# Optimization experiments

Hardware: AMD Instinct MI355X
Metric: run time of the kernel (lower is better)

The kernel has to match this reference:

```python
import jax, jax.numpy as jnp
import numpy as np

H_DIM = 256
NUM_HEADS = 8
HEAD_DIM = H_DIM // NUM_HEADS
BN_EPS = 1e-5
SCALE = float(np.sqrt(HEAD_DIM))


def _lens():
    # 512 graphs, ragged vertex counts cycling 32/64/96/128 -> 40960 total rows
    return np.tile(np.array([32, 64, 96, 128], dtype=np.int64), 128)


def _pad(x, lens):
    # gather ragged rows of x [total, D] into padded [B, Lmax, D]; mask [B, Lmax]
    B = lens.shape[0]
    L = int(lens.max())
    off = np.zeros(B, np.int64)
    off[1:] = np.cumsum(lens)[:-1]
    pos = np.arange(L)
    idx = off[:, None] + np.minimum(pos[None, :], lens[:, None] - 1)
    mask = pos[None, :] < lens[:, None]
    return x[jnp.asarray(idx)], jnp.asarray(mask)


def _flat_idx(lens):
    # (graph_id, position) for every real row, to un-pad back to ragged layout
    b = np.repeat(np.arange(lens.shape[0]), lens)
    i = np.concatenate([np.arange(int(l)) for l in lens])
    return jnp.asarray(b), jnp.asarray(i)


def _forward(src_h, dst_h, src_lens, dst_lens,
             W1, b1, gamma1, beta1, W2, b2, gamma2, beta2):
    src_pad, src_mask = _pad(src_h, src_lens)   # [B, Ls, H]
    dst_pad, _ = _pad(dst_h, dst_lens)          # [B, Ld, H]
    B, Ls, _ = src_pad.shape
    Ld = dst_pad.shape[1]
    # NOTE: original torch code zips self.proj but never applies it, so
    # q = raw dst, k = v = raw src.  The .view(1, head_dim, heads, N) on the
    # channel-major tensor splits feature f as f = d*NUM_HEADS + h.
    q = dst_pad.reshape(B, Ld, HEAD_DIM, NUM_HEADS)
    k = src_pad.reshape(B, Ls, HEAD_DIM, NUM_HEADS)
    v = k
    scores = jnp.einsum('bndh,bmdh->bhnm', q, k) / SCALE
    scores = jnp.where(src_mask[:, None, None, :], scores, jnp.float32(-1e30))
    attn = jax.nn.softmax(scores, axis=-1)
    out = jnp.einsum('bhnm,bmdh->bndh', attn, v).reshape(B, Ld, H_DIM)
    bidx, iidx = _flat_idx(dst_lens)
    h_msg = out[bidx, iidx]                     # [total_dst, H] ragged again
    h = dst_h
    z = jnp.concatenate([h, h_msg], axis=-1)    # [N, 2H]
    y = z @ W1.T + b1
    y = gamma1 * (y - y.mean(0)) * jax.lax.rsqrt(y.var(0) + BN_EPS) + beta1
    y = jax.nn.relu(y)
    y = y @ W2.T + b2
    y = gamma2 * (y - y.mean(0)) * jax.lax.rsqrt(y.var(0) + BN_EPS) + beta2
    return h + y


def setup_inputs() -> dict:
    lens = _lens()
    N = int(lens.sum())
    ks = jax.random.split(jax.random.key(0), 4)
    return {
        'src_h': jax.random.normal(ks[0], (N, H_DIM), jnp.float32),
        'dst_h': jax.random.normal(ks[1], (N, H_DIM), jnp.float32),
        'src_num_verts': jnp.asarray(lens, jnp.int32),
        'dst_num_verts': jnp.asarray(lens, jnp.int32),
        'W1': jax.random.normal(ks[2], (H_DIM, 2 * H_DIM), jnp.float32) / np.float32(np.sqrt(2 * H_DIM)),
        'b1': jnp.zeros((H_DIM,), jnp.float32),
        'gamma1': jnp.ones((H_DIM,), jnp.float32),
        'beta1': jnp.zeros((H_DIM,), jnp.float32),
        'W2': jax.random.normal(ks[3], (H_DIM, H_DIM), jnp.float32) / np.float32(np.sqrt(H_DIM)),
        'b2': jnp.zeros((H_DIM,), jnp.float32),
        'gamma2': jnp.ones((H_DIM,), jnp.float32),
        'beta2': jnp.zeros((H_DIM,), jnp.float32),
    }


def reference(src_h, dst_h, src_num_verts, dst_num_verts,
              W1, b1, gamma1, beta1, W2, b2, gamma2, beta2):
    # segment lengths are static metadata (torch.split takes a Python list)
    src_lens = np.asarray(jax.device_get(src_num_verts), np.int64)
    dst_lens = np.asarray(jax.device_get(dst_num_verts), np.int64)
    return _forward(src_h, dst_h, src_lens, dst_lens,
                    W1, b1, gamma1, beta1, W2, b2, gamma2, beta2)
```

## Files before the change

### kernel.cpp

```cpp
#include <hip/hip_runtime.h>
#include <cstddef>

#define H 256
#define NHEADS 8
#define HD 32

typedef __attribute__((ext_vector_type(8))) short bf16x8;
typedef __attribute__((ext_vector_type(4))) float f32x4;

__device__ __forceinline__ float bf2f(unsigned short s) {
    unsigned u = ((unsigned)s) << 16; return __builtin_bit_cast(float, u);
}
__device__ __forceinline__ float bfe2f(short s) {
    unsigned u = ((unsigned)(unsigned short)s) << 16; return __builtin_bit_cast(float, u);
}
__device__ __forceinline__ unsigned short f2bf(float x) {
    unsigned u = __builtin_bit_cast(unsigned, x);
    u += 0x7fffu + ((u >> 16) & 1u);
    return (unsigned short)(u >> 16);
}
__device__ __forceinline__ void gl_lds16(const void* g, void* l) {
    __builtin_amdgcn_global_load_lds(
        (const __attribute__((address_space(1))) void*)g,
        (__attribute__((address_space(3))) void*)l, 16, 0, 0);
}

__global__ __launch_bounds__(512) void scan_zero_kernel(
    const int* __restrict__ slen, const int* __restrict__ dlen,
    int* __restrict__ soff, int* __restrict__ doff,
    float* __restrict__ stats, int B)
{
    __shared__ int ss[512], dd[512];
    const int t = threadIdx.x;
    const int sv = (t < B) ? slen[t] : 0;
    const int dv = (t < B) ? dlen[t] : 0;
    ss[t] = sv; dd[t] = dv;
    __syncthreads();
    for (int o = 1; o < 512; o <<= 1) {
        int a = (t >= o) ? ss[t - o] : 0;
        int b = (t >= o) ? dd[t - o] : 0;
        __syncthreads();
        ss[t] += a; dd[t] += b;
        __syncthreads();
    }
    if (t < B) { soff[t] = ss[t] - sv; doff[t] = dd[t] - dv; }
    stats[t] = 0.f;
    stats[t + 512] = 0.f;
}

__global__ __launch_bounds__(256) void prepass_kernel(
    const float* __restrict__ src, const float* __restrict__ dst,
    unsigned short* __restrict__ KT, unsigned short* __restrict__ VT2,
    unsigned short* __restrict__ QT, int N)
{
    __shared__ unsigned short pl[8 * 64 * 40];
    const int t = threadIdx.x;
    const int rb = blockIdx.x * 64;
    const int isrc = (blockIdx.y == 0);
    const float* __restrict__ in = isrc ? src : dst;
    unsigned short* __restrict__ T = isrc ? KT : QT;
    #pragma unroll
    for (int i = 0; i < 16; ++i) {
        const int idx = t + i * 256;
        const int row = idx >> 6, f4 = idx & 63;
        const float4 v = ((const float4*)in)[(size_t)(rb + row) * 64 + f4];
        const int f0 = f4 * 4, h0 = f0 & 7, d = f0 >> 3;
        pl[(h0 + 0) * 2560 + row * 40 + d] = f2bf(v.x);
        pl[(h0 + 1) * 2560 + row * 40 + d] = f2bf(v.y);
        pl[(h0 + 2) * 2560 + row * 40 + d] = f2bf(v.z);
        pl[(h0 + 3) * 2560 + row * 40 + d] = f2bf(v.w);
    }
    __syncthreads();
    #pragma unroll
    for (int i = 0; i < 8; ++i) {
        const int idx = t + i * 256;
        const int h = idx >> 8, rem = idx & 255, row = rem >> 2, c = rem & 3;
        const bf16x8 val = *(const bf16x8*)&pl[h * 2560 + row * 40 + c * 8];
        *(bf16x8*)&T[(size_t)(h * N + rb + row) * 32 + c * 8] = val;
    }
    if (isrc) {
        #pragma unroll
        for (int i = 0; i < 8; ++i) {
            const int idx = t + i * 256;
            const int h = idx >> 8, rem = idx & 255, d = rem >> 3, nc = rem & 7;
            unsigned short tmp[8];
            #pragma unroll
            for (int j = 0; j < 8; ++j) tmp[j] = pl[h * 2560 + (nc * 8 + j) * 40 + d];
            ushort4 lo, hi;
            lo.x = tmp[0]; lo.y = tmp[1]; lo.z = tmp[2]; lo.w = tmp[3];
            hi.x = tmp[4]; hi.y = tmp[5]; hi.z = tmp[6]; hi.w = tmp[7];
            *(ushort4*)&VT2[(size_t)(h * 32 + d) * N + rb + nc * 8] = lo;
            *(ushort4*)&VT2[(size_t)(h * 32 + d) * N + rb + nc * 8 + 4] = hi;
        }
    }
}

__global__ __launch_bounds__(256) void cvtW_kernel(
    const float* __restrict__ W1, const float* __restrict__ W2,
    unsigned short* __restrict__ W1p, unsigned short* __restrict__ W2bf)
{
    const int idx = blockIdx.x * 256 + threadIdx.x;
    if (idx < 131072) {
        const int kp = idx & 511, c = idx >> 9;
        const int half = kp >> 8, r = kp & 255, hh = r >> 5, d = r & 31;
        W1p[(size_t)c * 512 + kp] = f2bf(W1[(size_t)c * 512 + half * 256 + d * 8 + hh]);
    } else {
        const int i2 = idx - 131072;
        W2bf[i2] = f2bf(W2[i2]);
    }
}

template<int LS>
__device__ __forceinline__ void attn_body(
    const unsigned short* __restrict__ KT, const unsigned short* __restrict__ QT,
    const unsigned short* __restrict__ VT2, unsigned short* __restrict__ OT,
    unsigned short* __restrict__ Ps, int N, int so, int df, int Ld, int h, int lane)
{
    constexpr int MT = LS / 16, CH = LS / 32;
    const int lr = lane & 15, lq = lane >> 4;
    const float iscale = 0.17677669529663687f;

    bf16x8 kf[MT];
    #pragma unroll
    for (int mt = 0; mt < MT; ++mt)
        kf[mt] = *(const bf16x8*)&KT[(size_t)(h * N + so + mt * 16 + lr) * 32 + lq * 8];
    bf16x8 vf[CH][2];
    #pragma unroll
    for (int c = 0; c < CH; ++c)
        #pragma unroll
        for (int dt = 0; dt < 2; ++dt)
            vf[c][dt] = *(const bf16x8*)&VT2[(size_t)(h * 32 + dt * 16 + lr) * N + so + c * 32 + lq * 8];

    const int NT = Ld >> 4;
    for (int nt = 0; nt < NT; ++nt) {
        const bf16x8 qf = *(const bf16x8*)&QT[(size_t)(h * N + df + nt * 16 + lr) * 32 + lq * 8];
        f32x4 s[MT];
        #pragma unroll
        for (int mt = 0; mt < MT; ++mt) {
            f32x4 z = {0.f, 0.f, 0.f, 0.f};
            s[mt] = __builtin_amdgcn_mfma_f32_16x16x32_bf16(kf[mt], qf, z, 0, 0, 0);
        }
        float mx = -INFINITY;
        #pragma unroll
        for (int mt = 0; mt < MT; ++mt)
            mx = fmaxf(mx, fmaxf(fmaxf(s[mt][0], s[mt][1]), fmaxf(s[mt][2], s[mt][3])));
        mx = fmaxf(mx, __shfl_xor(mx, 16));
        mx = fmaxf(mx, __shfl_xor(mx, 32));
        const float mxi = mx * iscale;
        float sum = 0.f;
        #pragma unroll
        for (int mt = 0; mt < MT; ++mt) {
            #pragma unroll
            for (int r = 0; r < 4; ++r) {
                const float e = __expf(s[mt][r] * iscale - mxi);
                s[mt][r] = e; sum += e;
            }
        }
        sum += __shfl_xor(sum, 16);
        sum += __shfl_xor(sum, 32);
        const float rinv = 1.f / sum;
        #pragma unroll
        for (int mt = 0; mt < MT; ++mt) {
            uint2 p;
            p.x = ((unsigned)f2bf(s[mt][0])) | (((unsigned)f2bf(s[mt][1])) << 16);
            p.y = ((unsigned)f2bf(s[mt][2])) | (((unsigned)f2bf(s[mt][3])) << 16);
            *(uint2*)&Ps[lr * 136 + mt * 16 + lq * 4] = p;
        }
        __asm__ volatile("" ::: "memory");
        __builtin_amdgcn_wave_barrier();
        f32x4 o0 = {0.f, 0.f, 0.f, 0.f}, o1 = {0.f, 0.f, 0.f, 0.f};
        #pragma unroll
        for (int c = 0; c < CH; ++c) {
            const bf16x8 pa = *(const bf16x8*)&Ps[lr * 136 + c * 32 + lq * 8];
            o0 = __builtin_amdgcn_mfma_f32_16x16x32_bf16(pa, vf[c][0], o0, 0, 0, 0);
            o1 = __builtin_amdgcn_mfma_f32_16x16x32_bf16(pa, vf[c][1], o1, 0, 0, 0);
        }
        __asm__ volatile("" ::: "memory");
        __builtin_amdgcn_wave_barrier();
        #pragma unroll
        for (int r = 0; r < 4; ++r) {
            const float rv = __shfl(rinv, lq * 4 + r);
            const int row = df + nt * 16 + lq * 4 + r;
            OT[(size_t)(h * N + row) * 32 + lr]      = f2bf(o0[r] * rv);
            OT[(size_t)(h * N + row) * 32 + 16 + lr] = f2bf(o1[r] * rv);
        }
    }
}

__global__ __launch_bounds__(256) void attn_mfma(
    const unsigned short* __restrict__ KT, const unsigned short* __restrict__ QT,
    const unsigned short* __restrict__ VT2, unsigned short* __restrict__ OT,
    const int* __restrict__ soff, const int* __restrict__ doff,
    const int* __restrict__ slen, const int* __restrict__ dlen, int N)
{
    __shared__ unsigned short Ps[4][16 * 136];
    const int b = blockIdx.x >> 1, half = blockIdx.x & 1;
    const int w = threadIdx.x >> 6, lane = threadIdx.x & 63;
    const int h = half * 4 + w;
    const int Ls = slen[b], Ld = dlen[b], so = soff[b], df = doff[b];
    switch (Ls) {
        case 32:  attn_body<32> (KT, QT, VT2, OT, Ps[w], N, so, df, Ld, h, lane); break;
        case 64:  attn_body<64> (KT, QT, VT2, OT, Ps[w], N, so, df, Ld, h, lane); break;
        case 96:  attn_body<96> (KT, QT, VT2, OT, Ps[w], N, so, df, Ld, h, lane); break;
        default:  attn_body<128>(KT, QT, VT2, OT, Ps[w], N, so, df, Ld, h, lane); break;
    }
}

__global__ __launch_bounds__(256) void gemm1_mfma(
    const unsigned short* __restrict__ QT, const unsigned short* __restrict__ OT,
    const unsigned short* __restrict__ W, const float* __restrict__ bias,
    unsigned short* __restrict__ out, float* __restrict__ sum, float* __restrict__ sq,
    int N)
{
    __shared__ unsigned short Abuf[2][8 * 512];
    __shared__ unsigned short Bbuf[2][8 * 512];
    const int tid = threadIdx.x;
    const int w = tid >> 6, lane = tid & 63;
    const int rowBase = blockIdx.y * 128, colBase = blockIdx.x * 128;
    const int lr = lane & 15, lq = lane >> 4;
    const int wm = w >> 1, wn = w & 1;

    f32x4 acc[4][4];
    #pragma unroll
    for (int i = 0; i < 4; ++i)
        #pragma unroll
        for (int j = 0; j < 4; ++j) { f32x4 z = {0.f, 0.f, 0.f, 0.f}; acc[i][j] = z; }

    auto stage = [&](int ks, int bi) {
        const unsigned short* __restrict__ Ap = (ks < 8) ? QT : OT;
        const int hh = ks & 7;
        #pragma unroll
        for (int s = 0; s < 2; ++s) {
            const int sub = 2 * w + s;
            gl_lds16(Ap + (size_t)(hh * N + rowBase + sub * 16 + lr) * 32 + lq * 8,
                     &Abuf[bi][sub * 512]);
            gl_lds16(W + (size_t)(colBase + sub * 16 + lr) * 512 + ks * 32 + lq * 8,
                     &Bbuf[bi][sub * 512]);
        }
    };
    auto compute = [&](int bi) {
        bf16x8 af[4], bfr[4];
        #pragma unroll
        for (int i = 0; i < 4; ++i) af[i] = *(const bf16x8*)&Abuf[bi][(wm * 4 + i) * 512 + lane * 8];
        #pragma unroll
        for (int j = 0; j < 4; ++j) bfr[j] = *(const bf16x8*)&Bbuf[bi][(wn * 4 + j) * 512 + lane * 8];
        #pragma unroll
        for (int i = 0; i < 4; ++i)
            #pragma unroll
            for (int j = 0; j < 4; ++j)
                acc[i][j] = __builtin_amdgcn_mfma_f32_16x16x32_bf16(af[i], bfr[j], acc[i][j], 0, 0, 0);
    };

    stage(0, 0);
    __syncthreads();
    for (int ks = 0; ks < 16; ks += 2) {
        stage(ks + 1, 1);
        compute(0);
        __syncthreads();
        if (ks + 2 < 16) stage(ks + 2, 0);
        compute(1);
        __syncthreads();
    }

    const int col0 = colBase + wn * 64;
    #pragma unroll
    for (int j = 0; j < 4; ++j) {
        const int col = col0 + j * 16 + lr;
        const float bv = bias[col];
        float cs = 0.f, cq = 0.f;
        #pragma unroll
        for (int i = 0; i < 4; ++i) {
            const int row0 = rowBase + wm * 64 + i * 16 + lq * 4;
            #pragma unroll
            for (int r = 0; r < 4; ++r) {
                const float v = acc[i][j][r] + bv;
                cs += v; cq += v * v;
                out[(size_t)(row0 + r) * 256 + col] = f2bf(v);
            }
        }
        cs += __shfl_xor(cs, 16); cs += __shfl_xor(cs, 32);
        cq += __shfl_xor(cq, 16); cq += __shfl_xor(cq, 32);
        if (lq == 0) { atomicAdd(&sum[col], cs); atomicAdd(&sq[col], cq); }
    }
}

__global__ __launch_bounds__(256) void gemm2_mfma(
    const unsigned short* __restrict__ A2,
    const unsigned short* __restrict__ W, const float* __restrict__ bias,
    unsigned short* __restrict__ out, float* __restrict__ sum, float* __restrict__ sq)
{
    __shared__ unsigned short Abuf[2][8 * 512];
    __shared__ unsigned short Bbuf[2][8 * 512];
    const int tid = threadIdx.x;
    const int w = tid >> 6, lane = tid & 63;
    const int rowBase = blockIdx.y * 128, colBase = blockIdx.x * 128;
    const int lr = lane & 15, lq = lane >> 4;
    const int wm = w >> 1, wn = w & 1;

    f32x4 acc[4][4];
    #pragma unroll
    for (int i = 0; i < 4; ++i)
        #pragma unroll
        for (int j = 0; j < 4; ++j) { f32x4 z = {0.f, 0.f, 0.f, 0.f}; acc[i][j] = z; }

    auto stage = [&](int ks, int bi) {
        #pragma unroll
        for (int s = 0; s < 2; ++s) {
            const int sub = 2 * w + s;
            gl_lds16(A2 + (size_t)(rowBase + sub * 16 + lr) * 256 + ks * 32 + lq * 8,
                     &Abuf[bi][sub * 512]);
            gl_lds16(W + (size_t)(colBase + sub * 16 + lr) * 256 + ks * 32 + lq * 8,
                     &Bbuf[bi][sub * 512]);
        }
    };
    auto compute = [&](int bi) {
        bf16x8 af[4], bfr[4];
        #pragma unroll
        for (int i = 0; i < 4; ++i) af[i] = *(const bf16x8*)&Abuf[bi][(wm * 4 + i) * 512 + lane * 8];
        #pragma unroll
        for (int j = 0; j < 4; ++j) bfr[j] = *(const bf16x8*)&Bbuf[bi][(wn * 4 + j) * 512 + lane * 8];
        #pragma unroll
        for (int i = 0; i < 4; ++i)
            #pragma unroll
            for (int j = 0; j < 4; ++j)
                acc[i][j] = __builtin_amdgcn_mfma_f32_16x16x32_bf16(af[i], bfr[j], acc[i][j], 0, 0, 0);
    };

    stage(0, 0);
    __syncthreads();
    for (int ks = 0; ks < 8; ks += 2) {
        stage(ks + 1, 1);
        compute(0);
        __syncthreads();
        if (ks + 2 < 8) stage(ks + 2, 0);
        compute(1);
        __syncthreads();
    }

    const int col0 = colBase + wn * 64;
    #pragma unroll
    for (int j = 0; j < 4; ++j) {
        const int col = col0 + j * 16 + lr;
        const float bv = bias[col];
        float cs = 0.f, cq = 0.f;
        #pragma unroll
        for (int i = 0; i < 4; ++i) {
            const int row0 = rowBase + wm * 64 + i * 16 + lq * 4;
            #pragma unroll
            for (int r = 0; r < 4; ++r) {
                const float v = acc[i][j][r] + bv;
                cs += v; cq += v * v;
                out[(size_t)(row0 + r) * 256 + col] = f2bf(v);
            }
        }
        cs += __shfl_xor(cs, 16); cs += __shfl_xor(cs, 32);
        cq += __shfl_xor(cq, 16); cq += __shfl_xor(cq, 32);
        if (lq == 0) { atomicAdd(&sum[col], cs); atomicAdd(&sq[col], cq); }
    }
}

__global__ __launch_bounds__(256) void bnrelu_kernel(
    const unsigned short* __restrict__ y1,
    const float* __restrict__ sum, const float* __restrict__ sq,
    const float* __restrict__ gamma, const float* __restrict__ beta,
    unsigned short* __restrict__ out, int n8, float invN)
{
    const int i = blockIdx.x * 256 + threadIdx.x;
    if (i >= n8) return;
    const int j0 = (i & 31) * 8;
    const bf16x8 yv = ((const bf16x8*)y1)[i];
    short res[8];
    #pragma unroll
    for (int j = 0; j < 8; ++j) {
        const float mean = sum[j0 + j] * invN;
        const float var  = sq[j0 + j] * invN - mean * mean;
        const float rstd = rsqrtf(var + 1e-5f);
        const float sc = gamma[j0 + j] * rstd;
        const float sh = beta[j0 + j] - mean * sc;
        res[j] = (short)f2bf(fmaxf(bfe2f(yv[j]) * sc + sh, 0.f));
    }
    bf16x8 o;
    #pragma unroll
    for (int j = 0; j < 8; ++j) o[j] = res[j];
    ((bf16x8*)out)[i] = o;
}

__global__ __launch_bounds__(256) void epilogue_kernel(
    const float* __restrict__ dst, const unsigned short* __restrict__ y2,
    const float* __restrict__ sum, const float* __restrict__ sq,
    const float* __restrict__ gamma, const float* __restrict__ beta,
    float* __restrict__ out, int n8, float invN)
{
    const int i = blockIdx.x * 256 + threadIdx.x;
    if (i >= n8) return;
    const int j0 = (i & 31) * 8;
    const bf16x8 yv = ((const bf16x8*)y2)[i];
    const float4 d0 = ((const float4*)dst)[2 * i];
    const float4 d1 = ((const float4*)dst)[2 * i + 1];
    float o[8];
    const float dv[8] = {d0.x, d0.y, d0.z, d0.w, d1.x, d1.y, d1.z, d1.w};
    #pragma unroll
    for (int j = 0; j < 8; ++j) {
        const float mean = sum[j0 + j] * invN;
        const float var  = sq[j0 + j] * invN - mean * mean;
        const float rstd = rsqrtf(var + 1e-5f);
        const float sc = gamma[j0 + j] * rstd;
        const float sh = beta[j0 + j] - mean * sc;
        o[j] = dv[j] + bfe2f(yv[j]) * sc + sh;
    }
    float4 o0, o1;
    o0.x = o[0]; o0.y = o[1]; o0.z = o[2]; o0.w = o[3];
    o1.x = o[4]; o1.y = o[5]; o1.z = o[6]; o1.w = o[7];
    ((float4*)out)[2 * i]     = o0;
    ((float4*)out)[2 * i + 1] = o1;
}

extern "C" void kernel_launch(void* const* d_in, const int* in_sizes, int n_in,
                              void* d_out, int out_size, void* d_ws, size_t ws_size,
                              hipStream_t stream)
{
    const float* src_h  = (const float*)d_in[0];
    const float* dst_h  = (const float*)d_in[1];
    const int*   slen   = (const int*)d_in[2];
    const int*   dlen   = (const int*)d_in[3];
    const float* W1     = (const float*)d_in[4];
    const float* b1     = (const float*)d_in[5];
    const float* gamma1 = (const float*)d_in[6];
    const float* beta1  = (const float*)d_in[7];
    const float* W2     = (const float*)d_in[8];
    const float* b2     = (const float*)d_in[9];
    const float* gamma2 = (const float*)d_in[10];
    const float* beta2  = (const float*)d_in[11];
    float* out = (float*)d_out;

    const int N = in_sizes[1] / H;
    const int B = in_sizes[2];

    char* base = (char*)d_ws;
    int*   soff   = (int*)(base + 0);
    int*   doff   = (int*)(base + 2048);
    float* stats  = (float*)(base + 4096);
    unsigned short* W1p  = (unsigned short*)(base + 16384);
    unsigned short* W2bf = (unsigned short*)(base + 16384 + 262144);
    const size_t S = (size_t)N * H * sizeof(unsigned short);
    char* big = base + (1 << 20);
    unsigned short* KT  = (unsigned short*)(big);
    unsigned short* VT2 = (unsigned short*)(big + S);
    unsigned short* QT  = (unsigned short*)(big + 2 * S);
    unsigned short* OT  = (unsigned short*)(big + 3 * S);
    unsigned short* y1bf = KT;
    unsigned short* a2   = VT2;
    unsigned short* y2bf = QT;

    const float invN = 1.0f / (float)N;

    scan_zero_kernel<<<1, 512, 0, stream>>>(slen, dlen, soff, doff, stats, B);

    prepass_kernel<<<dim3(N / 64, 2), 256, 0, stream>>>(src_h, dst_h, KT, VT2, QT, N);
    cvtW_kernel<<<768, 256, 0, stream>>>(W1, W2, W1p, W2bf);

    attn_mfma<<<B * 2, 256, 0, stream>>>(KT, QT, VT2, OT, soff, doff, slen, dlen, N);

    dim3 ggrid(H / 128, N / 128);
    gemm1_mfma<<<ggrid, 256, 0, stream>>>(QT, OT, W1p, b1, y1bf, stats + 0, stats + 256, N);

    const int n8 = N * H / 8;
    bnrelu_kernel<<<(n8 + 255) / 256, 256, 0, stream>>>(
        y1bf, stats + 0, stats + 256, gamma1, beta1, a2, n8, invN);

    gemm2_mfma<<<ggrid, 256, 0, stream>>>(a2, W2bf, b2, y2bf, stats + 512, stats + 768);

    epilogue_kernel<<<(n8 + 255) / 256, 256, 0, stream>>>(
        dst_h, y2bf, stats + 512, stats + 768, gamma2, beta2, out, n8, invN);
}
```

Before: 281.2 us.

## Shrink GEMM row tiles, prefetch Q fragments, reorder attention blocks, pad LDS planes

Both GEMM kernels now use 64x128 tiles instead of 128x128, doubling the grid, with each wave covering all 64 rows and 32 columns. The aim is better occupancy and more blocks across CUs. The attention kernel maps blocks so the largest graphs are scheduled first, and it prefetches the next Q fragment one iteration ahead. The prepass pads the LDS head-plane stride to cut bank conflicts and writes VT2 with one 16-byte store. Smaller GEMM tiles lower per-block reuse of W, so W traffic through LDS goes up.

Measured after the change: 276.0 us. Within noise of the previous version (-1.8%).

```diff
diff --git a/kernel.cpp b/kernel.cpp
--- a/kernel.cpp
+++ b/kernel.cpp
@@ -48,12 +48,13 @@
     stats[t + 512] = 0.f;
 }
 
+#define PS 2568
 __global__ __launch_bounds__(256) void prepass_kernel(
     const float* __restrict__ src, const float* __restrict__ dst,
     unsigned short* __restrict__ KT, unsigned short* __restrict__ VT2,
     unsigned short* __restrict__ QT, int N)
 {
-    __shared__ unsigned short pl[8 * 64 * 40];
+    __shared__ unsigned short pl[8 * PS];
     const int t = threadIdx.x;
     const int rb = blockIdx.x * 64;
     const int isrc = (blockIdx.y == 0);
@@ -65,17 +66,17 @@
         const int row = idx >> 6, f4 = idx & 63;
         const float4 v = ((const float4*)in)[(size_t)(rb + row) * 64 + f4];
         const int f0 = f4 * 4, h0 = f0 & 7, d = f0 >> 3;
-        pl[(h0 + 0) * 2560 + row * 40 + d] = f2bf(v.x);
-        pl[(h0 + 1) * 2560 + row * 40 + d] = f2bf(v.y);
-        pl[(h0 + 2) * 2560 + row * 40 + d] = f2bf(v.z);
-        pl[(h0 + 3) * 2560 + row * 40 + d] = f2bf(v.w);
+        pl[(h0 + 0) * PS + row * 40 + d] = f2bf(v.x);
+        pl[(h0 + 1) * PS + row * 40 + d] = f2bf(v.y);
+        pl[(h0 + 2) * PS + row * 40 + d] = f2bf(v.z);
+        pl[(h0 + 3) * PS + row * 40 + d] = f2bf(v.w);
     }
     __syncthreads();
     #pragma unroll
     for (int i = 0; i < 8; ++i) {
         const int idx = t + i * 256;
         const int h = idx >> 8, rem = idx & 255, row = rem >> 2, c = rem & 3;
-        const bf16x8 val = *(const bf16x8*)&pl[h * 2560 + row * 40 + c * 8];
+        const bf16x8 val = *(const bf16x8*)&pl[h * PS + row * 40 + c * 8];
         *(bf16x8*)&T[(size_t)(h * N + rb + row) * 32 + c * 8] = val;
     }
     if (isrc) {
@@ -83,14 +84,11 @@
         for (int i = 0; i < 8; ++i) {
             const int idx = t + i * 256;
             const int h = idx >> 8, rem = idx & 255, d = rem >> 3, nc = rem & 7;
-            unsigned short tmp[8];
-            #pragma unroll
-            for (int j = 0; j < 8; ++j) tmp[j] = pl[h * 2560 + (nc * 8 + j) * 40 + d];
-            ushort4 lo, hi;
-            lo.x = tmp[0]; lo.y = tmp[1]; lo.z = tmp[2]; lo.w = tmp[3];
-            hi.x = tmp[4]; hi.y = tmp[5]; hi.z = tmp[6]; hi.w = tmp[7];
-            *(ushort4*)&VT2[(size_t)(h * 32 + d) * N + rb + nc * 8] = lo;
-            *(ushort4*)&VT2[(size_t)(h * 32 + d) * N + rb + nc * 8 + 4] = hi;
+            bf16x8 v8;
+            #pragma unroll
+            for (int j = 0; j < 8; ++j)
+                v8[j] = (short)pl[h * PS + (nc * 8 + j) * 40 + d];
+            *(bf16x8*)&VT2[(size_t)(h * 32 + d) * N + rb + nc * 8] = v8;
         }
     }
 }
@@ -132,8 +130,11 @@
             vf[c][dt] = *(const bf16x8*)&VT2[(size_t)(h * 32 + dt * 16 + lr) * N + so + c * 32 + lq * 8];
 
     const int NT = Ld >> 4;
+    bf16x8 qf = *(const bf16x8*)&QT[(size_t)(h * N + df + lr) * 32 + lq * 8];
     for (int nt = 0; nt < NT; ++nt) {
-        const bf16x8 qf = *(const bf16x8*)&QT[(size_t)(h * N + df + nt * 16 + lr) * 32 + lq * 8];
+        bf16x8 qn = qf;
+        if (nt + 1 < NT)
+            qn = *(const bf16x8*)&QT[(size_t)(h * N + df + (nt + 1) * 16 + lr) * 32 + lq * 8];
         f32x4 s[MT];
         #pragma unroll
         for (int mt = 0; mt < MT; ++mt) {
@@ -184,6 +185,7 @@
             OT[(size_t)(h * N + row) * 32 + lr]      = f2bf(o0[r] * rv);
             OT[(size_t)(h * N + row) * 32 + 16 + lr] = f2bf(o1[r] * rv);
         }
+        qf = qn;
     }
 }
 
@@ -194,7 +196,9 @@
     const int* __restrict__ slen, const int* __restrict__ dlen, int N)
 {
     __shared__ unsigned short Ps[4][16 * 136];
-    const int b = blockIdx.x >> 1, half = blockIdx.x & 1;
+    const int i = blockIdx.x >> 1, half = blockIdx.x & 1;
+    const int grp = i >> 7, j = i & 127;
+    const int b = 4 * j + (3 - grp);
     const int w = threadIdx.x >> 6, lane = threadIdx.x & 63;
     const int h = half * 4 + w;
     const int Ls = slen[b], Ld = dlen[b], so = soff[b], df = doff[b];
@@ -212,42 +216,41 @@
     unsigned short* __restrict__ out, float* __restrict__ sum, float* __restrict__ sq,
     int N)
 {
-    __shared__ unsigned short Abuf[2][8 * 512];
+    __shared__ unsigned short Abuf[2][4 * 512];
     __shared__ unsigned short Bbuf[2][8 * 512];
     const int tid = threadIdx.x;
     const int w = tid >> 6, lane = tid & 63;
-    const int rowBase = blockIdx.y * 128, colBase = blockIdx.x * 128;
+    const int rowBase = blockIdx.y * 64, colBase = blockIdx.x * 128;
     const int lr = lane & 15, lq = lane >> 4;
-    const int wm = w >> 1, wn = w & 1;
-
-    f32x4 acc[4][4];
+
+    f32x4 acc[4][2];
     #pragma unroll
     for (int i = 0; i < 4; ++i)
         #pragma unroll
-        for (int j = 0; j < 4; ++j) { f32x4 z = {0.f, 0.f, 0.f, 0.f}; acc[i][j] = z; }
+        for (int j = 0; j < 2; ++j) { f32x4 z = {0.f, 0.f, 0.f, 0.f}; acc[i][j] = z; }
 
     auto stage = [&](int ks, int bi) {
         const unsigned short* __restrict__ Ap = (ks < 8) ? QT : OT;
         const int hh = ks & 7;
+        gl_lds16(Ap + (size_t)(hh * N + rowBase + w * 16 + lr) * 32 + lq * 8,
+                 &Abuf[bi][w * 512]);
         #pragma unroll
         for (int s = 0; s < 2; ++s) {
             const int sub = 2 * w + s;
-            gl_lds16(Ap + (size_t)(hh * N + rowBase + sub * 16 + lr) * 32 + lq * 8,
-                     &Abuf[bi][sub * 512]);
             gl_lds16(W + (size_t)(colBase + sub * 16 + lr) * 512 + ks * 32 + lq * 8,
                      &Bbuf[bi][sub * 512]);
         }
     };
     auto compute = [&](int bi) {
-        bf16x8 af[4], bfr[4];
-        #pragma unroll
-        for (int i = 0; i < 4; ++i) af[i] = *(const bf16x8*)&Abuf[bi][(wm * 4 + i) * 512 + lane * 8];
-        #pragma unroll
-        for (int j = 0; j < 4; ++j) bfr[j] = *(const bf16x8*)&Bbuf[bi][(wn * 4 + j) * 512 + lane * 8];
+        bf16x8 af[4], bfr[2];
+        #pragma unroll
+        for (int i = 0; i < 4; ++i) af[i] = *(const bf16x8*)&Abuf[bi][i * 512 + lane * 8];
+        #pragma unroll
+        for (int j = 0; j < 2; ++j) bfr[j] = *(const bf16x8*)&Bbuf[bi][(w * 2 + j) * 512 + lane * 8];
         #pragma unroll
         for (int i = 0; i < 4; ++i)
             #pragma unroll
-            for (int j = 0; j < 4; ++j)
+            for (int j = 0; j < 2; ++j)
                 acc[i][j] = __builtin_amdgcn_mfma_f32_16x16x32_bf16(af[i], bfr[j], acc[i][j], 0, 0, 0);
     };
 
@@ -262,15 +265,15 @@
         __syncthreads();
     }
 
-    const int col0 = colBase + wn * 64;
-    #pragma unroll
-    for (int j = 0; j < 4; ++j) {
+    const int col0 = colBase + w * 32;
+    #pragma unroll
+    for (int j = 0; j < 2; ++j) {
         const int col = col0 + j * 16 + lr;
         const float bv = bias[col];
         float cs = 0.f, cq = 0.f;
         #pragma unroll
         for (int i = 0; i < 4; ++i) {
-            const int row0 = rowBase + wm * 64 + i * 16 + lq * 4;
+            const int row0 = rowBase + i * 16 + lq * 4;
             #pragma unroll
             for (int r = 0; r < 4; ++r) {
                 const float v = acc[i][j][r] + bv;
@@ -289,40 +292,39 @@
     const unsigned short* __restrict__ W, const float* __restrict__ bias,
     unsigned short* __restrict__ out, float* __restrict__ sum, float* __restrict__ sq)
 {
-    __shared__ unsigned short Abuf[2][8 * 512];
+    __shared__ unsigned short Abuf[2][4 * 512];
     __shared__ unsigned short Bbuf[2][8 * 512];
     const int tid = threadIdx.x;
     const int w = tid >> 6, lane = tid & 63;
-    const int rowBase = blockIdx.y * 128, colBase = blockIdx.x * 128;
+    const int rowBase = blockIdx.y * 64, colBase = blockIdx.x * 128;
     const int lr = lane & 15, lq = lane >> 4;
-    const int wm = w >> 1, wn = w & 1;
-
-    f32x4 acc[4][4];
+
+    f32x4 acc[4][2];
     #pragma unroll
     for (int i = 0; i < 4; ++i)
         #pragma unroll
-        for (int j = 0; j < 4; ++j) { f32x4 z = {0.f, 0.f, 0.f, 0.f}; acc[i][j] = z; }
+        for (int j = 0; j < 2; ++j) { f32x4 z = {0.f, 0.f, 0.f, 0.f}; acc[i][j] = z; }
 
     auto stage = [&](int ks, int bi) {
+        gl_lds16(A2 + (size_t)(rowBase + w * 16 + lr) * 256 + ks * 32 + lq * 8,
+                 &Abuf[bi][w * 512]);
         #pragma unroll
         for (int s = 0; s < 2; ++s) {
             const int sub = 2 * w + s;
-            gl_lds16(A2 + (size_t)(rowBase + sub * 16 + lr) * 256 + ks * 32 + lq * 8,
-                     &Abuf[bi][sub * 512]);
             gl_lds16(W + (size_t)(colBase + sub * 16 + lr) * 256 + ks * 32 + lq * 8,
                      &Bbuf[bi][sub * 512]);
         }
     };
     auto compute = [&](int bi) {
-        bf16x8 af[4], bfr[4];
-        #pragma unroll
-        for (int i = 0; i < 4; ++i) af[i] = *(const bf16x8*)&Abuf[bi][(wm * 4 + i) * 512 + lane * 8];
-        #pragma unroll
-        for (int j = 0; j < 4; ++j) bfr[j] = *(const bf16x8*)&Bbuf[bi][(wn * 4 + j) * 512 + lane * 8];
+        bf16x8 af[4], bfr[2];
+        #pragma unroll
+        for (int i = 0; i < 4; ++i) af[i] = *(const bf16x8*)&Abuf[bi][i * 512 + lane * 8];
+        #pragma unroll
+        for (int j = 0; j < 2; ++j) bfr[j] = *(const bf16x8*)&Bbuf[bi][(w * 2 + j) * 512 + lane * 8];
         #pragma unroll
         for (int i = 0; i < 4; ++i)
             #pragma unroll
-            for (int j = 0; j < 4; ++j)
+            for (int j = 0; j < 2; ++j)
                 acc[i][j] = __builtin_amdgcn_mfma_f32_16x16x32_bf16(af[i], bfr[j], acc[i][j], 0, 0, 0);
     };
 
@@ -337,15 +339,15 @@
         __syncthreads();
     }
 
-    const int col0 = colBase + wn * 64;
-    #pragma unroll
-    for (int j = 0; j < 4; ++j) {
+    const int col0 = colBase + w * 32;
+    #pragma unroll
+    for (int j = 0; j < 2; ++j) {
         const int col = col0 + j * 16 + lr;
         const float bv = bias[col];
         float cs = 0.f, cq = 0.f;
         #pragma unroll
         for (int i = 0; i < 4; ++i) {
-            const int row0 = rowBase + wm * 64 + i * 16 + lq * 4;
+            const int row0 = rowBase + i * 16 + lq * 4;
             #pragma unroll
             for (int r = 0; r < 4; ++r) {
                 const float v = acc[i][j][r] + bv;
@@ -461,7 +463,7 @@
 
     attn_mfma<<<B * 2, 256, 0, stream>>>(KT, QT, VT2, OT, soff, doff, slen, dlen, N);
 
-    dim3 ggrid(H / 128, N / 128);
+    dim3 ggrid(H / 128, N / 64);
     gemm1_mfma<<<ggrid, 256, 0, stream>>>(QT, OT, W1p, b1, y1bf, stats + 0, stats + 256, N);
 
     const int n8 = N * H / 8;
```

## Deepen GEMM prefetch with vmcnt waits, prefetch Q, reorder attention blocks, pad LDS

Applied to the files above, without the earlier changes.

Both GEMM kernels now keep two stages in flight and wait with explicit s_waitcnt vmcnt(4) plus raw barriers, replacing the full __syncthreads after each stage, so global-to-LDS loads overlap MFMA compute. The attention kernel prefetches the next Q fragment inside its loop and schedules the largest graphs first to balance the ragged work. The prepass pads its LDS plane stride to cut bank conflicts and writes V transposed as one 16-byte store. The hand-written vmcnt counts assume a fixed number of outstanding loads per stage and are fragile if the compiler reorders them.

After: 276.5 us. Within noise of the previous version (-1.7%).

```diff
diff --git a/kernel.cpp b/kernel.cpp
--- a/kernel.cpp
+++ b/kernel.cpp
@@ -48,12 +48,13 @@
     stats[t + 512] = 0.f;
 }
 
+#define PS 2568
 __global__ __launch_bounds__(256) void prepass_kernel(
     const float* __restrict__ src, const float* __restrict__ dst,
     unsigned short* __restrict__ KT, unsigned short* __restrict__ VT2,
     unsigned short* __restrict__ QT, int N)
 {
-    __shared__ unsigned short pl[8 * 64 * 40];
+    __shared__ unsigned short pl[8 * PS];
     const int t = threadIdx.x;
     const int rb = blockIdx.x * 64;
     const int isrc = (blockIdx.y == 0);
@@ -65,17 +66,17 @@
         const int row = idx >> 6, f4 = idx & 63;
         const float4 v = ((const float4*)in)[(size_t)(rb + row) * 64 + f4];
         const int f0 = f4 * 4, h0 = f0 & 7, d = f0 >> 3;
-        pl[(h0 + 0) * 2560 + row * 40 + d] = f2bf(v.x);
-        pl[(h0 + 1) * 2560 + row * 40 + d] = f2bf(v.y);
-        pl[(h0 + 2) * 2560 + row * 40 + d] = f2bf(v.z);
-        pl[(h0 + 3) * 2560 + row * 40 + d] = f2bf(v.w);
+        pl[(h0 + 0) * PS + row * 40 + d] = f2bf(v.x);
+        pl[(h0 + 1) * PS + row * 40 + d] = f2bf(v.y);
+        pl[(h0 + 2) * PS + row * 40 + d] = f2bf(v.z);
+        pl[(h0 + 3) * PS + row * 40 + d] = f2bf(v.w);
     }
     __syncthreads();
     #pragma unroll
     for (int i = 0; i < 8; ++i) {
         const int idx = t + i * 256;
         const int h = idx >> 8, rem = idx & 255, row = rem >> 2, c = rem & 3;
-        const bf16x8 val = *(const bf16x8*)&pl[h * 2560 + row * 40 + c * 8];
+        const bf16x8 val = *(const bf16x8*)&pl[h * PS + row * 40 + c * 8];
         *(bf16x8*)&T[(size_t)(h * N + rb + row) * 32 + c * 8] = val;
     }
     if (isrc) {
@@ -83,14 +84,11 @@
         for (int i = 0; i < 8; ++i) {
             const int idx = t + i * 256;
             const int h = idx >> 8, rem = idx & 255, d = rem >> 3, nc = rem & 7;
-            unsigned short tmp[8];
-            #pragma unroll
-            for (int j = 0; j < 8; ++j) tmp[j] = pl[h * 2560 + (nc * 8 + j) * 40 + d];
-            ushort4 lo, hi;
-            lo.x = tmp[0]; lo.y = tmp[1]; lo.z = tmp[2]; lo.w = tmp[3];
-            hi.x = tmp[4]; hi.y = tmp[5]; hi.z = tmp[6]; hi.w = tmp[7];
-            *(ushort4*)&VT2[(size_t)(h * 32 + d) * N + rb + nc * 8] = lo;
-            *(ushort4*)&VT2[(size_t)(h * 32 + d) * N + rb + nc * 8 + 4] = hi;
+            bf16x8 v8;
+            #pragma unroll
+            for (int j = 0; j < 8; ++j)
+                v8[j] = (short)pl[h * PS + (nc * 8 + j) * 40 + d];
+            *(bf16x8*)&VT2[(size_t)(h * 32 + d) * N + rb + nc * 8] = v8;
         }
     }
 }
@@ -132,8 +130,11 @@
             vf[c][dt] = *(const bf16x8*)&VT2[(size_t)(h * 32 + dt * 16 + lr) * N + so + c * 32 + lq * 8];
 
     const int NT = Ld >> 4;
+    bf16x8 qf = *(const bf16x8*)&QT[(size_t)(h * N + df + lr) * 32 + lq * 8];
     for (int nt = 0; nt < NT; ++nt) {
-        const bf16x8 qf = *(const bf16x8*)&QT[(size_t)(h * N + df + nt * 16 + lr) * 32 + lq * 8];
+        bf16x8 qn = qf;
+        if (nt + 1 < NT)
+            qn = *(const bf16x8*)&QT[(size_t)(h * N + df + (nt + 1) * 16 + lr) * 32 + lq * 8];
         f32x4 s[MT];
         #pragma unroll
         for (int mt = 0; mt < MT; ++mt) {
@@ -184,6 +185,7 @@
             OT[(size_t)(h * N + row) * 32 + lr]      = f2bf(o0[r] * rv);
             OT[(size_t)(h * N + row) * 32 + 16 + lr] = f2bf(o1[r] * rv);
         }
+        qf = qn;
     }
 }
 
@@ -194,7 +196,9 @@
     const int* __restrict__ slen, const int* __restrict__ dlen, int N)
 {
     __shared__ unsigned short Ps[4][16 * 136];
-    const int b = blockIdx.x >> 1, half = blockIdx.x & 1;
+    const int i = blockIdx.x >> 1, half = blockIdx.x & 1;
+    const int grp = i >> 7, j = i & 127;
+    const int b = 4 * j + (3 - grp);
     const int w = threadIdx.x >> 6, lane = threadIdx.x & 63;
     const int h = half * 4 + w;
     const int Ls = slen[b], Ld = dlen[b], so = soff[b], df = doff[b];
@@ -252,14 +256,16 @@
     };
 
     stage(0, 0);
-    __syncthreads();
-    for (int ks = 0; ks < 16; ks += 2) {
-        stage(ks + 1, 1);
-        compute(0);
-        __syncthreads();
-        if (ks + 2 < 16) stage(ks + 2, 0);
-        compute(1);
-        __syncthreads();
+    stage(1, 1);
+    #pragma unroll
+    for (int ks = 0; ks < 16; ++ks) {
+        if (ks < 15) asm volatile("s_waitcnt vmcnt(4)" ::: "memory");
+        else         asm volatile("s_waitcnt vmcnt(0)" ::: "memory");
+        __builtin_amdgcn_s_barrier();
+        compute(ks & 1);
+        asm volatile("s_waitcnt lgkmcnt(0)" ::: "memory");
+        __builtin_amdgcn_s_barrier();
+        if (ks + 2 < 16) stage(ks + 2, ks & 1);
     }
 
     const int col0 = colBase + wn * 64;
@@ -327,14 +333,16 @@
     };
 
     stage(0, 0);
-    __syncthreads();
-    for (int ks = 0; ks < 8; ks += 2) {
-        stage(ks + 1, 1);
-        compute(0);
-        __syncthreads();
-        if (ks + 2 < 8) stage(ks + 2, 0);
-        compute(1);
-        __syncthreads();
+    stage(1, 1);
+    #pragma unroll
+    for (int ks = 0; ks < 8; ++ks) {
+        if (ks < 7) asm volatile("s_waitcnt vmcnt(4)" ::: "memory");
+        else        asm volatile("s_waitcnt vmcnt(0)" ::: "memory");
+        __builtin_amdgcn_s_barrier();
+        compute(ks & 1);
+        asm volatile("s_waitcnt lgkmcnt(0)" ::: "memory");
+        __builtin_amdgcn_s_barrier();
+        if (ks + 2 < 8) stage(ks + 2, ks & 1);
     }
 
     const int col0 = colBase + wn * 64;
```
